# Optimization experiments

Hardware: AMD Instinct MI355X
Metric: run time of the kernel (lower is better)

## Reference

```python
import jax, jax.numpy as jnp
import numpy as np

NUM_FIELDS = 24
FIELD_DIM = 2000
VOCAB = NUM_FIELDS * FIELD_DIM  # sum(field_dims) = 48000
EMBED_DIM = 64
H1, H2 = 64, 32
NUM_INTERACTIONS = 16
BATCH = 4096


def setup_inputs() -> dict:
    key = jax.random.key(0)
    ks = jax.random.split(key, 12)
    s = 0.05  # xavier-ish scale
    return {
        "x": jax.random.randint(ks[0], (BATCH, NUM_FIELDS), 0, FIELD_DIM, dtype=jnp.int32),
        # per-field embedding tables stacked: (num_fields, vocab, embed_dim)
        "tables": jax.random.normal(ks[1], (NUM_FIELDS, VOCAB, EMBED_DIM), jnp.float32) * s,
        "fc_w": jax.random.normal(ks[2], (VOCAB, 1), jnp.float32) * s,
        "fc_b": jnp.zeros((1,), jnp.float32),
        "w1": jax.random.normal(ks[3], (2 * EMBED_DIM, H1), jnp.float32) * s,
        "b1": jnp.zeros((H1,), jnp.float32),
        "w2": jax.random.normal(ks[4], (H1, H2), jnp.float32) * s,
        "b2": jnp.zeros((H2,), jnp.float32),
        "w3": jax.random.normal(ks[5], (H2, 1), jnp.float32) * s,
        "b3": jnp.zeros((1,), jnp.float32),
        "proj_w": jax.random.normal(ks[6], (EMBED_DIM, 1), jnp.float32) * s,
        "proj_b": jnp.zeros((1,), jnp.float32),
        "bias": jnp.zeros((1,), jnp.float32),
    }


def reference(x, tables, fc_w, fc_b, w1, b1, w2, b2, w3, b3, proj_w, proj_b, bias):
    offsets = jnp.arange(NUM_FIELDS, dtype=x.dtype) * FIELD_DIM  # cumsum of equal field_dims
    idx = x + offsets[None, :]  # (B, F)

    # FeaturesLinear: first-order term, (B, 1)
    linear_part = fc_w[idx].sum(axis=1) + fc_b

    # FeaturesEmbedding: per-field table lookup -> (B, F, D)
    emb = tables[jnp.arange(NUM_FIELDS)[None, :], idx]

    # FeatureInteractionDetector: all i<j pairs, concat, score with MLP
    iu, ju = jnp.triu_indices(NUM_FIELDS, k=1)  # (P,), P = F*(F-1)/2
    pair_emb = jnp.concatenate([emb[:, iu], emb[:, ju]], axis=-1)  # (B, P, 2D)
    h = jax.nn.relu(pair_emb @ w1 + b1)
    h = jax.nn.relu(h @ w2 + b2)
    scores = (h @ w3 + b3)[..., 0]  # (B, P)

    # topk over batch-mean scores, gather per-sample scores and pair indices
    _, top = jax.lax.top_k(scores.mean(axis=0), NUM_INTERACTIONS)  # (K,)
    sel_scores = scores[:, top]  # (B, K)
    sel_i, sel_j = iu[top], ju[top]

    # FeatureCrossing: elementwise product of selected pairs, score-weighted sum, project
    crossed = emb[:, sel_i] * emb[:, sel_j]  # (B, K, D)
    summed = jnp.sum(crossed * sel_scores[..., None], axis=1)  # (B, D)
    crossed_part = summed @ proj_w + proj_b  # (B, 1)

    out = linear_part + crossed_part + bias  # (B, 1)
    return out[:, 0]
```

## Files before the change

### kernel.cpp

```cpp
#include <hip/hip_runtime.h>
#include <stdint.h>

#define NF 24
#define FD 2000
#define VOCABSZ 48000
#define ED 64
#define H1D 64
#define H2D 32
#define NPAIR 276
#define BATCH 4096
#define NSEL 16
#define NTILE 256
#define PBASE 49152

typedef _Float16 f16x8 __attribute__((ext_vector_type(8)));
typedef float f32x4 __attribute__((ext_vector_type(4)));

union U4 { f16x8 v; uint32_t u[4]; uint4 q; };

__device__ __forceinline__ uint32_t pkrtz(float lo, float hi){
  uint32_t r; asm("v_cvt_pkrtz_f16_f32 %0, %1, %2" : "=v"(r) : "v"(lo), "v"(hi)); return r;
}
__device__ __forceinline__ uint32_t pk_add(uint32_t a, uint32_t b){
  uint32_t r; asm("v_pk_add_f16 %0, %1, %2" : "=v"(r) : "v"(a), "v"(b)); return r;
}
__device__ __forceinline__ uint32_t pk_mul(uint32_t a, uint32_t b){
  uint32_t r; asm("v_pk_mul_f16 %0, %1, %2" : "=v"(r) : "v"(a), "v"(b)); return r;
}
__device__ __forceinline__ uint32_t pk_relu(uint32_t a){
  uint32_t r; asm("v_pk_max_f16 %0, %1, %2" : "=v"(r) : "v"(a), "v"(0u)); return r;
}
#define DPP_ADD(v, ctrl) \
  (v) += __int_as_float(__builtin_amdgcn_update_dpp(0, __float_as_int(v), (ctrl), 0xF, 0xF, true))

__global__ __launch_bounds__(1024) void k_pair(
    const int* __restrict__ x, const float* __restrict__ tables,
    const float* __restrict__ w1, const float* __restrict__ b1,
    const float* __restrict__ w2, const float* __restrict__ b2,
    const float* __restrict__ w3, const float* __restrict__ b3,
    const float* __restrict__ proj_w,
    float* __restrict__ sgarr, float* __restrict__ part){
  __shared__ __align__(16) char smem[147456];
  const int tid  = threadIdx.x;
  const int bt   = blockIdx.x;
  const int lane = tid & 63;
  const int w    = tid >> 6;
  const int n    = lane & 15;
  const int kg   = lane >> 4;

  const int half = w >> 3;
  const int oq   = (w >> 1) & 3;
  const int fg   = w & 1;
  const int isPt = (half == 0);
  const float b3v = b3[0];

  const int o = 16*oq + n;
  U4 wp0, wp1;
  {
    const float* wsrc = w1 + (size_t)(isPt ? 0 : ED)*H1D + o;
    #pragma unroll
    for(int j=0;j<8;j++) wp0.v[j] = (_Float16)wsrc[(kg*8+j)*H1D];
    #pragma unroll
    for(int j=0;j<8;j++) wp1.v[j] = (_Float16)wsrc[(32+kg*8+j)*H1D];
  }
  const float b1v = isPt ? b1[o] : 0.f;

  U4 wf[2][2];
  #pragma unroll
  for(int kh=0;kh<2;kh++)
    #pragma unroll
    for(int nh=0;nh<2;nh++)
      #pragma unroll
      for(int q2=0;q2<4;q2++){
        float lo = w2[(kg*8 + 2*q2     + 32*kh)*H2D + n + 16*nh];
        float hi = w2[(kg*8 + 2*q2 + 1 + 32*kh)*H2D + n + 16*nh];
        wf[kh][nh].u[q2] = pkrtz(lo, hi);
      }
  float b2r[2][4], w3r[2][4];
  #pragma unroll
  for(int oh=0;oh<2;oh++)
    #pragma unroll
    for(int r=0;r<4;r++){
      b2r[oh][r] = b2[16*oh + kg*4 + r];
      w3r[oh][r] = w3[16*oh + kg*4 + r];
    }

  float pwr[16];
  #pragma unroll
  for(int q=0;q<16;q++) pwr[q] = proj_w[kg*16 + q];

  #pragma unroll
  for(int i=0;i<3;i++){
    int c = i*1024 + tid;
    int rid = c >> 3;
    int qc = c & 7;
    int f = rid >> 4, b = rid & 15;
    int xv = x[(bt*16 + b)*NF + f];
    const float4* rp = (const float4*)(tables + ((size_t)f*VOCABSZ + (size_t)f*FD + (size_t)xv)*ED + qc*8);
    float4 v0 = rp[0], v1 = rp[1];
    uint4 pk;
    pk.x = pkrtz(v0.x, v0.y); pk.y = pkrtz(v0.z, v0.w);
    pk.z = pkrtz(v1.x, v1.y); pk.w = pkrtz(v1.z, v1.w);
    uint32_t db = ((uint32_t)(f*2048 + b*128 + qc*16)) ^ ((uint32_t)(b&7)<<4);
    *(uint4*)(smem + db) = pk;
  }
  __syncthreads();

  {
    const uint32_t rswz = ((uint32_t)(n&7))<<4;
    const int slab0 = isPt ? 0 : 24;
    for(int ff=0; ff<12; ff++){
      int f = fg*12 + ff;
      U4 a0, a1;
      a0.q = *(const uint4*)(smem + (((uint32_t)(f*2048 + n*128      + kg*16)) ^ rswz));
      a1.q = *(const uint4*)(smem + (((uint32_t)(f*2048 + n*128 + 64 + kg*16)) ^ rswz));
      f32x4 acc = {b1v, b1v, b1v, b1v};
      acc = __builtin_amdgcn_mfma_f32_16x16x32_f16(a0.v, wp0.v, acc, 0,0,0);
      acc = __builtin_amdgcn_mfma_f32_16x16x32_f16(a1.v, wp1.v, acc, 0,0,0);
      int sl = slab0 + f;
      #pragma unroll
      for(int r=0;r<4;r++){
        float up = __shfl_xor(acc[r], 1, 64);
        if((lane & 1) == 0){
          int bo = kg*4 + r;
          int k2 = 8*oq + (n>>1);
          uint32_t db = ((uint32_t)(PBASE + sl*2048 + bo*128 + k2*4)) ^ ((uint32_t)(bo&7)<<4);
          *(uint32_t*)(smem + db) = pkrtz(acc[r], up);
        }
      }
    }
  }
  __syncthreads();

  {
    int p0, np;
    if(w < 4){ np = 18; p0 = w*18; } else { np = 17; p0 = 72 + (w-4)*17; }
    int ii = 0, rem = p0;
    while(rem >= (NF-1-ii)){ rem -= (NF-1-ii); ii++; }
    int jj = ii + 1 + rem;

    const uint32_t aswz = ((uint32_t)(n&7))<<4;
    const uint32_t rowoff = (uint32_t)n*128;
    const uint32_t qoff = (uint32_t)kg*16;
    const uint32_t kg32 = (uint32_t)kg*32;

    int cached_i = -1;
    U4 ta0, ta1, ei0, ei1;

    for(int t=0;t<np;t++){
      int p = p0 + t;
      if(ii != cached_i){
        uint32_t tb = (uint32_t)(PBASE + ii*2048) + rowoff;
        ta0.q = *(const uint4*)(smem + ((tb + qoff     ) ^ aswz));
        ta1.q = *(const uint4*)(smem + ((tb + qoff + 64) ^ aswz));
        uint32_t ebi = (uint32_t)(ii*2048) + rowoff + kg32;
        ei0.q = *(const uint4*)(smem + ((ebi     ) ^ aswz));
        ei1.q = *(const uint4*)(smem + ((ebi + 16) ^ aswz));
        cached_i = ii;
      }
      uint32_t ub = (uint32_t)(PBASE + (24+jj)*2048) + rowoff;
      uint4 c0 = *(const uint4*)(smem + ((ub + qoff     ) ^ aswz));
      uint4 c1 = *(const uint4*)(smem + ((ub + qoff + 64) ^ aswz));
      uint32_t ebj = (uint32_t)(jj*2048) + rowoff + kg32;
      U4 ej0, ej1;
      ej0.q = *(const uint4*)(smem + ((ebj     ) ^ aswz));
      ej1.q = *(const uint4*)(smem + ((ebj + 16) ^ aswz));

      U4 h0, h1;
      h0.u[0]=pk_relu(pk_add(ta0.u[0],c0.x)); h0.u[1]=pk_relu(pk_add(ta0.u[1],c0.y));
      h0.u[2]=pk_relu(pk_add(ta0.u[2],c0.z)); h0.u[3]=pk_relu(pk_add(ta0.u[3],c0.w));
      h1.u[0]=pk_relu(pk_add(ta1.u[0],c1.x)); h1.u[1]=pk_relu(pk_add(ta1.u[1],c1.y));
      h1.u[2]=pk_relu(pk_add(ta1.u[2],c1.z)); h1.u[3]=pk_relu(pk_add(ta1.u[3],c1.w));

      f32x4 acc0 = {0.f,0.f,0.f,0.f}, acc1 = {0.f,0.f,0.f,0.f};
      acc0 = __builtin_amdgcn_mfma_f32_16x16x32_f16(wf[0][0].v, h0.v, acc0, 0,0,0);
      acc0 = __builtin_amdgcn_mfma_f32_16x16x32_f16(wf[1][0].v, h1.v, acc0, 0,0,0);
      acc1 = __builtin_amdgcn_mfma_f32_16x16x32_f16(wf[0][1].v, h0.v, acc1, 0,0,0);
      acc1 = __builtin_amdgcn_mfma_f32_16x16x32_f16(wf[1][1].v, h1.v, acc1, 0,0,0);

      U4 m0, m1;
      #pragma unroll
      for(int q=0;q<4;q++){ m0.u[q] = pk_mul(ei0.u[q], ej0.u[q]); m1.u[q] = pk_mul(ei1.u[q], ej1.u[q]); }
      float gp = 0.f;
      #pragma unroll
      for(int j=0;j<8;j++) gp += (float)m0.v[j]*pwr[j] + (float)m1.v[j]*pwr[8+j];
      gp += __shfl_xor(gp, 16, 64);
      gp += __shfl_xor(gp, 32, 64);

      float tsum = 0.f;
      #pragma unroll
      for(int r=0;r<4;r++){
        float v0 = acc0[r] + b2r[0][r]; v0 = v0>0.f?v0:0.f;
        float v1 = acc1[r] + b2r[1][r]; v1 = v1>0.f?v1:0.f;
        tsum += v0*w3r[0][r] + v1*w3r[1][r];
      }
      tsum += __shfl_xor(tsum, 16, 64);
      tsum += __shfl_xor(tsum, 32, 64);
      float sc = tsum + b3v;

      if(lane < 16) sgarr[(size_t)p*BATCH + bt*16 + lane] = sc * gp;

      float d = sc;
      DPP_ADD(d, 0x111);
      DPP_ADD(d, 0x112);
      DPP_ADD(d, 0x114);
      DPP_ADD(d, 0x118);
      if(lane == 15) part[(size_t)p*NTILE + bt] = d;

      if(++jj == NF){ ii++; jj = ii+1; }
    }
  }
}

__global__ __launch_bounds__(1024) void k_final(
    const int* __restrict__ x, const float* __restrict__ sgarr,
    const float* __restrict__ part,
    const float* __restrict__ fc_w, const float* __restrict__ fc_b,
    const float* __restrict__ proj_b, const float* __restrict__ bias,
    float* __restrict__ out){
  __shared__ float means[NPAIR];
  __shared__ int sel[NSEL];
  int tid = threadIdx.x;
  int bt = blockIdx.x;

  if(tid < NPAIR){
    const float4* pp = (const float4*)(part + (size_t)tid*NTILE);
    float4 s4 = {0.f,0.f,0.f,0.f};
    #pragma unroll 8
    for(int i=0;i<NTILE/4;i++){
      float4 v = pp[i];
      s4.x += v.x; s4.y += v.y; s4.z += v.z; s4.w += v.w;
    }
    means[tid] = (s4.x + s4.y) + (s4.z + s4.w);
  }
  __syncthreads();
  if(tid < 64){
    int l = tid;
    float v[5];
    #pragma unroll
    for(int q=0;q<5;q++){
      int i = l + q*64;
      v[q] = (i < NPAIR) ? means[i] : -3.0e38f;
    }
    for(int s=0;s<NSEL;s++){
      float bv = v[0]; int bslot = 0;
      #pragma unroll
      for(int q=1;q<5;q++){ if(v[q] > bv){ bv = v[q]; bslot = q; } }
      int bi = l + bslot*64;
      float cv = bv; int ci = bi;
      #pragma unroll
      for(int m=1;m<64;m<<=1){
        float ov = __shfl_xor(cv, m, 64);
        int   oi = __shfl_xor(ci, m, 64);
        if(ov > cv || (ov == cv && oi < ci)){ cv = ov; ci = oi; }
      }
      if(l == 0) sel[s] = ci;
      if(bi == ci) v[bslot] = -3.0e38f;
    }
  }
  __syncthreads();

  int row = tid >> 6, lane = tid & 63;
  int brow = bt*16 + row;
  float v = 0.f;
  if(lane < NSEL){
    v = sgarr[(size_t)sel[lane]*BATCH + brow];
  } else if(lane >= 32 && lane < 32+NF){
    int fl = lane - 32;
    v = fc_w[x[brow*NF + fl] + fl*FD];
  }
  #pragma unroll
  for(int m=1;m<64;m<<=1) v += __shfl_xor(v, m, 64);
  if(lane == 0) out[brow] = v + fc_b[0] + proj_b[0] + bias[0];
}

extern "C" void kernel_launch(void* const* d_in, const int* in_sizes, int n_in,
                              void* d_out, int out_size, void* d_ws, size_t ws_size,
                              hipStream_t stream){
  const int*   x      = (const int*)  d_in[0];
  const float* tables = (const float*)d_in[1];
  const float* fc_w   = (const float*)d_in[2];
  const float* fc_b   = (const float*)d_in[3];
  const float* w1     = (const float*)d_in[4];
  const float* b1     = (const float*)d_in[5];
  const float* w2     = (const float*)d_in[6];
  const float* b2     = (const float*)d_in[7];
  const float* w3     = (const float*)d_in[8];
  const float* b3     = (const float*)d_in[9];
  const float* proj_w = (const float*)d_in[10];
  const float* proj_b = (const float*)d_in[11];
  const float* bias   = (const float*)d_in[12];
  float* out = (float*)d_out;

  float* sgarr = (float*)d_ws;
  float* part  = sgarr + (size_t)NPAIR*BATCH;

  k_pair<<<NTILE, 1024, 0, stream>>>(x, tables, w1, b1, w2, b2, w3, b3, proj_w, sgarr, part);
  k_final<<<NTILE, 1024, 0, stream>>>(x, sgarr, part, fc_w, fc_b, proj_b, bias, out);
}
```

Baseline: 51.88 us.

## Transpose score buffer layout, use fdot2 for projection, parallelize mean reduction

```diff
diff --git a/kernel.cpp b/kernel.cpp
--- a/kernel.cpp
+++ b/kernel.cpp
@@ -14,9 +14,11 @@
 #define PBASE 49152
 
 typedef _Float16 f16x8 __attribute__((ext_vector_type(8)));
+typedef _Float16 f16x2 __attribute__((ext_vector_type(2)));
 typedef float f32x4 __attribute__((ext_vector_type(4)));
 
 union U4 { f16x8 v; uint32_t u[4]; uint4 q; };
+union H2U { f16x2 h; uint32_t u; };
 
 __device__ __forceinline__ uint32_t pkrtz(float lo, float hi){
   uint32_t r; asm("v_cvt_pkrtz_f16_f32 %0, %1, %2" : "=v"(r) : "v"(lo), "v"(hi)); return r;
@@ -29,6 +31,10 @@
 }
 __device__ __forceinline__ uint32_t pk_relu(uint32_t a){
   uint32_t r; asm("v_pk_max_f16 %0, %1, %2" : "=v"(r) : "v"(a), "v"(0u)); return r;
+}
+__device__ __forceinline__ float fdot2(uint32_t a, uint32_t b, float c){
+  H2U ua, ub; ua.u = a; ub.u = b;
+  return __builtin_amdgcn_fdot2(ua.h, ub.h, c, false);
 }
 #define DPP_ADD(v, ctrl) \
   (v) += __int_as_float(__builtin_amdgcn_update_dpp(0, __float_as_int(v), (ctrl), 0xF, 0xF, true))
@@ -39,7 +45,7 @@
     const float* __restrict__ w2, const float* __restrict__ b2,
     const float* __restrict__ w3, const float* __restrict__ b3,
     const float* __restrict__ proj_w,
-    float* __restrict__ sgarr, float* __restrict__ part){
+    float* __restrict__ sgT, float* __restrict__ part){
   __shared__ __align__(16) char smem[147456];
   const int tid  = threadIdx.x;
   const int bt   = blockIdx.x;
@@ -85,9 +91,9 @@
       w3r[oh][r] = w3[16*oh + kg*4 + r];
     }
 
-  float pwr[16];
-  #pragma unroll
-  for(int q=0;q<16;q++) pwr[q] = proj_w[kg*16 + q];
+  uint32_t pw2[8];
+  #pragma unroll
+  for(int j=0;j<8;j++) pw2[j] = pkrtz(proj_w[kg*16 + 2*j], proj_w[kg*16 + 2*j + 1]);
 
   #pragma unroll
   for(int i=0;i<3;i++){
@@ -120,13 +126,9 @@
       int sl = slab0 + f;
       #pragma unroll
       for(int r=0;r<4;r++){
-        float up = __shfl_xor(acc[r], 1, 64);
-        if((lane & 1) == 0){
-          int bo = kg*4 + r;
-          int k2 = 8*oq + (n>>1);
-          uint32_t db = ((uint32_t)(PBASE + sl*2048 + bo*128 + k2*4)) ^ ((uint32_t)(bo&7)<<4);
-          *(uint32_t*)(smem + db) = pkrtz(acc[r], up);
-        }
+        int bo = kg*4 + r;
+        uint32_t db = ((uint32_t)(PBASE + sl*2048 + bo*128 + o*2)) ^ (((uint32_t)(bo&7))<<4);
+        *(_Float16*)(smem + db) = (_Float16)acc[r];
       }
     }
   }
@@ -178,12 +180,11 @@
       acc1 = __builtin_amdgcn_mfma_f32_16x16x32_f16(wf[0][1].v, h0.v, acc1, 0,0,0);
       acc1 = __builtin_amdgcn_mfma_f32_16x16x32_f16(wf[1][1].v, h1.v, acc1, 0,0,0);
 
-      U4 m0, m1;
-      #pragma unroll
-      for(int q=0;q<4;q++){ m0.u[q] = pk_mul(ei0.u[q], ej0.u[q]); m1.u[q] = pk_mul(ei1.u[q], ej1.u[q]); }
       float gp = 0.f;
       #pragma unroll
-      for(int j=0;j<8;j++) gp += (float)m0.v[j]*pwr[j] + (float)m1.v[j]*pwr[8+j];
+      for(int q=0;q<4;q++) gp = fdot2(pk_mul(ei0.u[q], ej0.u[q]), pw2[q],   gp);
+      #pragma unroll
+      for(int q=0;q<4;q++) gp = fdot2(pk_mul(ei1.u[q], ej1.u[q]), pw2[4+q], gp);
       gp += __shfl_xor(gp, 16, 64);
       gp += __shfl_xor(gp, 32, 64);
 
@@ -198,7 +199,7 @@
       tsum += __shfl_xor(tsum, 32, 64);
       float sc = tsum + b3v;
 
-      if(lane < 16) sgarr[(size_t)p*BATCH + bt*16 + lane] = sc * gp;
+      if(lane < 16) sgT[(size_t)bt*(NPAIR*16) + p*16 + lane] = sc * gp;
 
       float d = sc;
       DPP_ADD(d, 0x111);
@@ -213,7 +214,7 @@
 }
 
 __global__ __launch_bounds__(1024) void k_final(
-    const int* __restrict__ x, const float* __restrict__ sgarr,
+    const int* __restrict__ x, const float* __restrict__ sgT,
     const float* __restrict__ part,
     const float* __restrict__ fc_w, const float* __restrict__ fc_b,
     const float* __restrict__ proj_b, const float* __restrict__ bias,
@@ -223,15 +224,33 @@
   int tid = threadIdx.x;
   int bt = blockIdx.x;
 
-  if(tid < NPAIR){
-    const float4* pp = (const float4*)(part + (size_t)tid*NTILE);
+  {
+    int p = tid >> 2, q = tid & 3;
+    const float4* pp = (const float4*)(part + (size_t)p*NTILE + q*64);
     float4 s4 = {0.f,0.f,0.f,0.f};
-    #pragma unroll 8
-    for(int i=0;i<NTILE/4;i++){
+    #pragma unroll
+    for(int i=0;i<16;i++){
       float4 v = pp[i];
       s4.x += v.x; s4.y += v.y; s4.z += v.z; s4.w += v.w;
     }
-    means[tid] = (s4.x + s4.y) + (s4.z + s4.w);
+    float s = (s4.x + s4.y) + (s4.z + s4.w);
+    s += __shfl_xor(s, 1, 64);
+    s += __shfl_xor(s, 2, 64);
+    if(q == 0 && p < 256) means[p] = s;
+    if(tid < 80){
+      int p2 = 256 + (tid >> 2);
+      const float4* pp2 = (const float4*)(part + (size_t)p2*NTILE + q*64);
+      float4 t4 = {0.f,0.f,0.f,0.f};
+      #pragma unroll
+      for(int i=0;i<16;i++){
+        float4 v = pp2[i];
+        t4.x += v.x; t4.y += v.y; t4.z += v.z; t4.w += v.w;
+      }
+      float s2 = (t4.x + t4.y) + (t4.z + t4.w);
+      s2 += __shfl_xor(s2, 1, 64);
+      s2 += __shfl_xor(s2, 2, 64);
+      if(q == 0) means[p2] = s2;
+    }
   }
   __syncthreads();
   if(tid < 64){
@@ -264,7 +283,7 @@
   int brow = bt*16 + row;
   float v = 0.f;
   if(lane < NSEL){
-    v = sgarr[(size_t)sel[lane]*BATCH + brow];
+    v = sgT[(size_t)bt*(NPAIR*16) + sel[lane]*16 + row];
   } else if(lane >= 32 && lane < 32+NF){
     int fl = lane - 32;
     v = fc_w[x[brow*NF + fl] + fl*FD];
@@ -292,9 +311,9 @@
   const float* bias   = (const float*)d_in[12];
   float* out = (float*)d_out;
 
-  float* sgarr = (float*)d_ws;
-  float* part  = sgarr + (size_t)NPAIR*BATCH;
-
-  k_pair<<<NTILE, 1024, 0, stream>>>(x, tables, w1, b1, w2, b2, w3, b3, proj_w, sgarr, part);
-  k_final<<<NTILE, 1024, 0, stream>>>(x, sgarr, part, fc_w, fc_b, proj_b, bias, out);
-}
+  float* sgT  = (float*)d_ws;
+  float* part = sgT + (size_t)NTILE*NPAIR*16;
+
+  k_pair<<<NTILE, 1024, 0, stream>>>(x, tables, w1, b1, w2, b2, w3, b3, proj_w, sgT, part);
+  k_final<<<NTILE, 1024, 0, stream>>>(x, sgT, part, fc_w, fc_b, proj_b, bias, out);
+}
```

New measurement: 48.52 us (median of 2 runs). 6.5% less time.
